# Kernel optimization log

Hardware: AMD Instinct MI355X
Metric: run time of the kernel (lower is better)

## Reference

```python
import jax, jax.numpy as jnp
import numpy as np

B, S, H = 1, 2048, 2048
NH, HD, RD = 32, 64, 64      # n_heads, head_dim, qk_mqa_dim (rope dim)
QR, KVR = 1024, 896          # q_lora_rank, kv_lora_rank
EPS = 1e-6
SCALE = HD ** -0.5           # scaling = head_dim ** -0.5 (as in module)


def rotate_half(x):
    x1, x2 = jnp.split(x, 2, axis=-1)
    return jnp.concatenate((-x2, x1), axis=-1)


def rmsnorm(x, w):
    var = jnp.mean(jnp.square(x), axis=-1, keepdims=True)
    return x * jax.lax.rsqrt(var + EPS) * w


def setup_inputs() -> dict:
    key = jax.random.key(0)
    ks = jax.random.split(key, 8)
    hidden_states = jax.random.normal(ks[0], (B, S, H), jnp.float32)
    # rotary tables over RD dims (applied only to the rope slice)
    inv_freq = 1.0 / (10000.0 ** (np.arange(0, RD, 2, dtype=np.float32) / RD))
    ang = np.arange(S, dtype=np.float32)[:, None] * inv_freq[None, :]
    emb = np.concatenate([ang, ang], axis=-1)  # [S, RD]
    cos = jnp.tile(jnp.asarray(np.cos(emb))[None], (B, 1, 1))
    sin = jnp.tile(jnp.asarray(np.sin(emb))[None], (B, 1, 1))
    s = 0.02
    q_a_w = s * jax.random.normal(ks[1], (QR, H), jnp.float32)
    q_a_ln_w = jnp.ones((QR,), jnp.float32)
    q_b_w = s * jax.random.normal(ks[2], (NH * (HD + RD), QR), jnp.float32)
    kv_a_w = s * jax.random.normal(ks[3], (KVR + RD, H), jnp.float32)
    kv_a_ln_w = jnp.ones((KVR,), jnp.float32)
    kv_b_w = s * jax.random.normal(ks[4], (NH * 2 * HD, KVR), jnp.float32)
    o_w = s * jax.random.normal(ks[5], (H, NH * HD), jnp.float32)
    return {"hidden_states": hidden_states, "cos": cos, "sin": sin,
            "q_a_w": q_a_w, "q_a_ln_w": q_a_ln_w, "q_b_w": q_b_w,
            "kv_a_w": kv_a_w, "kv_a_ln_w": kv_a_ln_w, "kv_b_w": kv_b_w,
            "o_w": o_w}


def reference(hidden_states, cos, sin, q_a_w, q_a_ln_w, q_b_w,
              kv_a_w, kv_a_ln_w, kv_b_w, o_w):
    b, s, _ = hidden_states.shape
    # Q: low-rank down -> RMSNorm -> up, split nope/rope per head
    q_lat = rmsnorm(hidden_states @ q_a_w.T, q_a_ln_w)             # [B,S,QR]
    q = (q_lat @ q_b_w.T).reshape(b, s, NH, HD + RD).transpose(0, 2, 1, 3)
    q_nope, q_rope = q[..., :HD], q[..., HD:]                      # [B,NH,S,HD/RD]
    # KV: joint down-proj with shared MQA rope key
    ckv = hidden_states @ kv_a_w.T                                 # [B,S,KVR+RD]
    c_kv, k_rope = ckv[..., :KVR], ckv[..., KVR:]
    k_rope = k_rope[:, None]                                       # [B,1,S,RD]
    kv = (rmsnorm(c_kv, kv_a_ln_w) @ kv_b_w.T).reshape(b, s, NH, 2 * HD)
    kv = kv.transpose(0, 2, 1, 3)                                  # [B,NH,S,2HD]
    k_nope, v = kv[..., :HD], kv[..., HD:]
    # RoPE on rope slices only (cos/sin unsqueezed over head dim)
    c_, s_ = cos[:, None], sin[:, None]
    q_rope = q_rope * c_ + rotate_half(q_rope) * s_
    k_rope = k_rope * c_ + rotate_half(k_rope) * s_
    q_full = jnp.concatenate([q_nope, q_rope], axis=-1)            # [B,NH,S,HD+RD]
    k_full = jnp.concatenate(
        [k_nope, jnp.broadcast_to(k_rope, (b, NH, s, RD))], axis=-1)
    # causal SDPA
    scores = jnp.einsum('bhqd,bhkd->bhqk', q_full, k_full) * SCALE
    mask = jnp.tril(jnp.ones((s, s), bool))
    scores = jnp.where(mask, scores, jnp.finfo(scores.dtype).min)
    attn = jax.nn.softmax(scores, axis=-1)
    out = jnp.einsum('bhqk,bhkd->bhqd', attn, v)                   # [B,NH,S,HD]
    out = out.transpose(0, 2, 1, 3).reshape(b, s, NH * HD)
    return out @ o_w.T                                             # [B,S,H]
```

## Files before the change

### kernel.cpp

```cpp
#include <hip/hip_runtime.h>


typedef __attribute__((ext_vector_type(8))) __bf16 bf16x8;
typedef __attribute__((ext_vector_type(4))) float f32x4;
typedef __attribute__((ext_vector_type(4))) unsigned u32x4;

__device__ __forceinline__ unsigned short f2bf(float f) {
  unsigned int x = __builtin_bit_cast(unsigned int, f);
  x += 0x7fffu + ((x >> 16) & 1u);
  return (unsigned short)(x >> 16);
}
__device__ __forceinline__ void gload_lds16(const void* g, void* l) {
  __builtin_amdgcn_global_load_lds(
      (const __attribute__((address_space(1))) void*)g,
      (__attribute__((address_space(3))) void*)l, 16, 0, 0);
}

struct CvtSegs {
  const float* src[6];
  unsigned short* dst[6];
  unsigned int n_src[6];
  unsigned int n_tot[6];
  unsigned int blk0[7];
};

__global__ __launch_bounds__(256) void cvt_all(CvtSegs sg) {
  int b = blockIdx.x;
  int seg = 0;
#pragma unroll
  for (int k = 0; k < 5; ++k)
    if (b >= (int)sg.blk0[k + 1]) seg = k + 1;
  size_t i = ((size_t)(b - sg.blk0[seg]) * 256 + threadIdx.x) * 4;
  if (i >= sg.n_tot[seg]) return;
  unsigned short o0 = 0, o1 = 0, o2 = 0, o3 = 0;
  if (i < sg.n_src[seg]) {
    float4 v = *reinterpret_cast<const float4*>(sg.src[seg] + i);
    o0 = f2bf(v.x); o1 = f2bf(v.y); o2 = f2bf(v.z); o3 = f2bf(v.w);
  }
  *reinterpret_cast<ushort4*>(sg.dst[seg] + i) = make_ushort4(o0, o1, o2, o3);
}

__global__ __launch_bounds__(512, 4) void gemm_bt2(const unsigned short* __restrict__ A,
                                                   const unsigned short* __restrict__ B,
                                                   float* __restrict__ C,
                                                   int M, int N, int K) {
  __shared__ unsigned short lA0[128 * 64], lA1[128 * 64];
  __shared__ unsigned short lB0[64 * 64], lB1[64 * 64];
  const int tid = threadIdx.x, lane = tid & 63, wv = tid >> 6;
  const int wr = wv >> 1, wc = wv & 1;
  const int bm = blockIdx.y * 128, bn = blockIdx.x * 64;

  f32x4 acc[2][2] = {};

  const int ar0 = tid >> 3;
  const int acol = (((tid & 7) ^ ((tid >> 3) & 7))) * 8;
  const int swz = lane & 7;

  auto stage = [&](unsigned short* la, unsigned short* lb, int k0) {
#pragma unroll
    for (int i = 0; i < 2; ++i)
      gload_lds16(A + (size_t)(bm + i * 64 + ar0) * K + k0 + acol,
                  &la[(i * 512 + wv * 64) * 8]);
    gload_lds16(B + (size_t)(bn + ar0) * K + k0 + acol, &lb[(wv * 64) * 8]);
  };

  auto compute = [&](const unsigned short* la, const unsigned short* lb) {
#pragma unroll
    for (int ks = 0; ks < 2; ++ks) {
      const int ch = ((ks * 4 + (lane >> 4)) ^ swz) * 8;
      bf16x8 af[2], bfr[2];
#pragma unroll
      for (int m = 0; m < 2; ++m)
        af[m] = *reinterpret_cast<const bf16x8*>(
            &la[(wr * 32 + m * 16 + (lane & 15)) * 64 + ch]);
#pragma unroll
      for (int n = 0; n < 2; ++n)
        bfr[n] = *reinterpret_cast<const bf16x8*>(
            &lb[(wc * 32 + n * 16 + (lane & 15)) * 64 + ch]);
      __builtin_amdgcn_s_setprio(1);
#pragma unroll
      for (int m = 0; m < 2; ++m)
#pragma unroll
        for (int n = 0; n < 2; ++n)
          acc[m][n] = __builtin_amdgcn_mfma_f32_16x16x32_bf16(af[m], bfr[n], acc[m][n], 0, 0, 0);
      __builtin_amdgcn_s_setprio(0);
    }
  };

  stage(lA0, lB0, 0);
  for (int k0 = 0; k0 < K; k0 += 128) {
    __syncthreads();
    stage(lA1, lB1, k0 + 64);
    compute(lA0, lB0);
    __syncthreads();
    if (k0 + 128 < K) stage(lA0, lB0, k0 + 128);
    compute(lA1, lB1);
  }

  const int r0 = bm + wr * 32, c0 = bn + wc * 32;
#pragma unroll
  for (int m = 0; m < 2; ++m)
#pragma unroll
    for (int n = 0; n < 2; ++n)
#pragma unroll
      for (int r = 0; r < 4; ++r)
        C[(size_t)(r0 + m * 16 + (lane >> 4) * 4 + r) * N + c0 + n * 16 + (lane & 15)] =
            acc[m][n][r];
}

__global__ __launch_bounds__(256) void rmsnorm_rope(const float* __restrict__ C1,
                                                    const float* __restrict__ qw,
                                                    const float* __restrict__ kvw,
                                                    const float* __restrict__ cosp,
                                                    const float* __restrict__ sinp,
                                                    unsigned short* __restrict__ qn,
                                                    unsigned short* __restrict__ ckvn,
                                                    unsigned short* __restrict__ kr) {
  const int s = blockIdx.x, tid = threadIdx.x;
  const float* row = C1 + (size_t)s * 2048;
  __shared__ float red[4];

  float4 v = *reinterpret_cast<const float4*>(row + tid * 4);
  float ss = v.x * v.x + v.y * v.y + v.z * v.z + v.w * v.w;
  ss += __shfl_xor(ss, 32); ss += __shfl_xor(ss, 16); ss += __shfl_xor(ss, 8);
  ss += __shfl_xor(ss, 4);  ss += __shfl_xor(ss, 2);  ss += __shfl_xor(ss, 1);
  if ((tid & 63) == 0) red[tid >> 6] = ss;
  __syncthreads();
  float rs = rsqrtf((red[0] + red[1] + red[2] + red[3]) * (1.f / 1024.f) + 1e-6f);
  {
    float4 w = *reinterpret_cast<const float4*>(qw + tid * 4);
    *reinterpret_cast<ushort4*>(qn + (size_t)s * 1024 + tid * 4) =
        make_ushort4(f2bf(v.x * rs * w.x), f2bf(v.y * rs * w.y),
                     f2bf(v.z * rs * w.z), f2bf(v.w * rs * w.w));
  }

  float4 u = make_float4(0.f, 0.f, 0.f, 0.f);
  if (tid < 224) u = *reinterpret_cast<const float4*>(row + 1024 + tid * 4);
  ss = u.x * u.x + u.y * u.y + u.z * u.z + u.w * u.w;
  ss += __shfl_xor(ss, 32); ss += __shfl_xor(ss, 16); ss += __shfl_xor(ss, 8);
  ss += __shfl_xor(ss, 4);  ss += __shfl_xor(ss, 2);  ss += __shfl_xor(ss, 1);
  __syncthreads();
  if ((tid & 63) == 0) red[tid >> 6] = ss;
  __syncthreads();
  rs = rsqrtf((red[0] + red[1] + red[2] + red[3]) * (1.f / 896.f) + 1e-6f);
  if (tid < 224) {
    float4 w = *reinterpret_cast<const float4*>(kvw + tid * 4);
    *reinterpret_cast<ushort4*>(ckvn + (size_t)s * 896 + tid * 4) =
        make_ushort4(f2bf(u.x * rs * w.x), f2bf(u.y * rs * w.y),
                     f2bf(u.z * rs * w.z), f2bf(u.w * rs * w.w));
  }

  if (tid < 64) {
    int d = tid;
    float x = row[1920 + d];
    float part = (d < 32) ? -row[1920 + d + 32] : row[1920 + d - 32];
    float vv = x * cosp[(size_t)s * 64 + d] + part * sinp[(size_t)s * 64 + d];
    kr[(size_t)s * 64 + d] = f2bf(vv);
  }
}

__global__ __launch_bounds__(256) void q_post(const float* __restrict__ Qf,
                                              const float* __restrict__ cosp,
                                              const float* __restrict__ sinp,
                                              unsigned short* __restrict__ Qb) {
  size_t base = ((size_t)blockIdx.x * 256 + threadIdx.x) * 4;
  int s = (int)(base >> 12);
  int w = (int)(base & 127);
  float4 x = *reinterpret_cast<const float4*>(Qf + base);
  float4 o;
  if (w < 64) {
    o = x;
  } else {
    int d = w - 64;
    float sgn = (d < 32) ? -1.f : 1.f;
    float4 prt = (d < 32) ? *reinterpret_cast<const float4*>(Qf + base + 32)
                          : *reinterpret_cast<const float4*>(Qf + base - 32);
    float4 c = *reinterpret_cast<const float4*>(cosp + (size_t)s * 64 + d);
    float4 sn = *reinterpret_cast<const float4*>(sinp + (size_t)s * 64 + d);
    o.x = x.x * c.x + sgn * prt.x * sn.x;
    o.y = x.y * c.y + sgn * prt.y * sn.y;
    o.z = x.z * c.z + sgn * prt.z * sn.z;
    o.w = x.w * c.w + sgn * prt.w * sn.w;
  }
  const float SC = 0.18033688f;
  *reinterpret_cast<ushort4*>(Qb + base) =
      make_ushort4(f2bf(o.x * SC), f2bf(o.y * SC), f2bf(o.z * SC), f2bf(o.w * SC));
}

__global__ __launch_bounds__(256) void kv_post(const float* __restrict__ KVf,
                                               const unsigned short* __restrict__ kr,
                                               unsigned short* __restrict__ Kb,
                                               unsigned short* __restrict__ Vt) {
  __shared__ float lT[64 * 65];
  const int s0 = blockIdx.x * 64, h = blockIdx.y, tid = threadIdx.x;
  for (int idx = tid; idx < 4096; idx += 256) {
    int r = idx >> 6, c = idx & 63;
    size_t base = (size_t)(s0 + r) * 4096 + h * 128;
    Kb[base + c] = f2bf(KVf[base + c]);
    Kb[base + 64 + c] = kr[(size_t)(s0 + r) * 64 + c];
    lT[r * 65 + c] = KVf[base + 64 + c];
  }
  __syncthreads();
  for (int idx = tid; idx < 4096; idx += 256) {
    int d = idx >> 6, c = idx & 63;
    Vt[((size_t)h * 64 + d) * 2048 + s0 + c] = f2bf(lT[c * 65 + d]);
  }
}

__global__ __launch_bounds__(256, 4) void flash_attn(const unsigned short* __restrict__ Qb,
                                                     const unsigned short* __restrict__ Kb,
                                                     const unsigned short* __restrict__ Vt,
                                                     unsigned short* __restrict__ Ao) {
  __shared__ unsigned short lK0[64 * 128], lK1[64 * 128];
  const int tid = threadIdx.x, lane = tid & 63, wv = tid >> 6;
  const int h = blockIdx.x;
  const int qb = (int)gridDim.y - 1 - (int)blockIdx.y;
  const int q0 = qb * 64;
  const int nt = qb + 1;
  const int firstrow = q0 + wv * 16;
  const int qa = firstrow + (lane & 15);

  bf16x8 qf[4];
  {
    const unsigned short* qrow = Qb + (size_t)(firstrow + (lane & 15)) * 4096 + h * 128;
#pragma unroll
    for (int ks = 0; ks < 4; ++ks)
      qf[ks] = *reinterpret_cast<const bf16x8*>(qrow + ks * 32 + (lane >> 4) * 8);
  }

  f32x4 o_acc[4] = {};
  float mrow = -1e30f, lrow = 0.f;

  const int g = lane >> 4;
  const int sl0 = ((g & 1) * 2) * 16 + (lane & 15);
  const int sl1 = sl0 + 16;
  const bool hi = g >= 2;

  const int krow = wv * 4 + (lane >> 4);
  const int kcol = (((lane & 15) ^ (krow & 7)) * 8);
  const int swz = lane & 7;

  auto stage = [&](int t, unsigned short* lK) {
    int j0 = t * 64;
#pragma unroll
    for (int i = 0; i < 4; ++i)
      gload_lds16(Kb + (size_t)(j0 + i * 16 + krow) * 4096 + h * 128 + kcol,
                  &lK[(i * 16 + wv * 4) * 128]);
  };

  auto loadV = [&](int j0, bf16x8 (&vr)[2][4]) {
#pragma unroll
    for (int ks = 0; ks < 2; ++ks)
#pragma unroll
      for (int n = 0; n < 4; ++n)
        vr[ks][n] = *reinterpret_cast<const bf16x8*>(
            Vt + ((size_t)h * 64 + n * 16 + (lane & 15)) * 2048 + j0 + ks * 32 +
            (lane >> 4) * 8);
  };

  auto computeT = [&](int j0, const unsigned short* lK, const bf16x8 (&vr)[2][4]) {
    f32x4 sT[4] = {};
    __builtin_amdgcn_s_setprio(1);
#pragma unroll
    for (int n = 0; n < 4; ++n)
#pragma unroll
      for (int ks = 0; ks < 4; ++ks) {
        bf16x8 kf = *reinterpret_cast<const bf16x8*>(
            &lK[(n * 16 + (lane & 15)) * 128 + (((ks * 4 + (lane >> 4)) ^ swz)) * 8]);
        sT[n] = __builtin_amdgcn_mfma_f32_16x16x32_bf16(kf, qf[ks], sT[n], 0, 0, 0);
      }
    __builtin_amdgcn_s_setprio(0);

    if (j0 == q0) {
#pragma unroll
      for (int n = 0; n < 4; ++n)
#pragma unroll
        for (int r = 0; r < 4; ++r) {
          int key = j0 + n * 16 + g * 4 + r;
          if (key > qa) sT[n][r] = -1e30f;
        }
    }

    float mx = sT[0][0];
#pragma unroll
    for (int n = 0; n < 4; ++n)
#pragma unroll
      for (int r = 0; r < 4; ++r) mx = fmaxf(mx, sT[n][r]);
    mx = fmaxf(mx, __shfl_xor(mx, 16));
    mx = fmaxf(mx, __shfl_xor(mx, 32));

    if (__any(mx - mrow > 8.0f)) {
      float mn = fmaxf(mrow, mx);
      float sf = exp2f(mrow - mn);
      mrow = mn;
      lrow *= sf;
      float sfr[4];
#pragma unroll
      for (int r = 0; r < 4; ++r) sfr[r] = __shfl(sf, (lane >> 4) * 4 + r);
#pragma unroll
      for (int n = 0; n < 4; ++n)
#pragma unroll
        for (int r = 0; r < 4; ++r) o_acc[n][r] *= sfr[r];
    }

    float ps = 0.f;
    unsigned dw[4][2];
#pragma unroll
    for (int n = 0; n < 4; ++n) {
      float p0 = exp2f(sT[n][0] - mrow), p1 = exp2f(sT[n][1] - mrow);
      float p2 = exp2f(sT[n][2] - mrow), p3 = exp2f(sT[n][3] - mrow);
      ps += (p0 + p1) + (p2 + p3);
      asm("v_cvt_pk_bf16_f32 %0, %1, %2" : "=v"(dw[n][0]) : "v"(p0), "v"(p1));
      asm("v_cvt_pk_bf16_f32 %0, %1, %2" : "=v"(dw[n][1]) : "v"(p2), "v"(p3));
    }
    ps += __shfl_xor(ps, 16);
    ps += __shfl_xor(ps, 32);
    lrow += ps;

#pragma unroll
    for (int ks = 0; ks < 2; ++ks) {
      unsigned A0 = __shfl(dw[2 * ks][0], sl0);
      unsigned B0 = __shfl(dw[2 * ks + 1][0], sl0);
      unsigned A1 = __shfl(dw[2 * ks][1], sl0);
      unsigned B1 = __shfl(dw[2 * ks + 1][1], sl0);
      unsigned A2 = __shfl(dw[2 * ks][0], sl1);
      unsigned B2 = __shfl(dw[2 * ks + 1][0], sl1);
      unsigned A3 = __shfl(dw[2 * ks][1], sl1);
      unsigned B3 = __shfl(dw[2 * ks + 1][1], sl1);
      u32x4 mm;
      mm.x = hi ? B0 : A0; mm.y = hi ? B1 : A1;
      mm.z = hi ? B2 : A2; mm.w = hi ? B3 : A3;
      bf16x8 pa = __builtin_bit_cast(bf16x8, mm);
      __builtin_amdgcn_s_setprio(1);
#pragma unroll
      for (int n = 0; n < 4; ++n)
        o_acc[n] = __builtin_amdgcn_mfma_f32_16x16x32_bf16(pa, vr[ks][n], o_acc[n], 0, 0, 0);
      __builtin_amdgcn_s_setprio(0);
    }
  };

  bf16x8 vr[2][4];
  stage(0, lK0);
  for (int t = 0; t < nt; t += 2) {
    __syncthreads();
    if (t + 1 < nt) stage(t + 1, lK1);
    loadV(t * 64, vr);
    computeT(t * 64, lK0, vr);
    if (t + 1 < nt) {
      __syncthreads();
      if (t + 2 < nt) stage(t + 2, lK0);
      loadV((t + 1) * 64, vr);
      computeT((t + 1) * 64, lK1, vr);
    }
  }

  float inv = 1.f / lrow;
  float invr[4];
#pragma unroll
  for (int r = 0; r < 4; ++r) invr[r] = __shfl(inv, (lane >> 4) * 4 + r);
#pragma unroll
  for (int n = 0; n < 4; ++n)
#pragma unroll
    for (int r = 0; r < 4; ++r) {
      float o = o_acc[n][r] * invr[r];
      Ao[(size_t)(firstrow + (lane >> 4) * 4 + r) * 2048 + h * 64 + n * 16 + (lane & 15)] =
          f2bf(o);
    }
}

extern "C" void kernel_launch(void* const* d_in, const int* in_sizes, int n_in,
                              void* d_out, int out_size, void* d_ws, size_t ws_size,
                              hipStream_t stream) {
  const float* hs   = (const float*)d_in[0];
  const float* cosp = (const float*)d_in[1];
  const float* sinp = (const float*)d_in[2];
  const float* qaw  = (const float*)d_in[3];
  const float* qaln = (const float*)d_in[4];
  const float* qbwf = (const float*)d_in[5];
  const float* kvaw = (const float*)d_in[6];
  const float* kvln = (const float*)d_in[7];
  const float* kvbwf= (const float*)d_in[8];
  const float* owf  = (const float*)d_in[9];
  float* out = (float*)d_out;
  char* ws = (char*)d_ws;
  const size_t MB = 1u << 20;

  unsigned short* W1b  = (unsigned short*)(ws + 0);
  unsigned short* Ao   = (unsigned short*)(ws + 0);
  unsigned short* qbw  = (unsigned short*)(ws + 8 * MB);
  unsigned short* Vt   = (unsigned short*)(ws + 8 * MB);
  unsigned short* kvbw = (unsigned short*)(ws + 16 * MB);
  unsigned short* owb  = (unsigned short*)(ws + 23 * MB);
  unsigned short* hsb  = (unsigned short*)(ws + 31 * MB);
  unsigned short* Qb   = (unsigned short*)(ws + 31 * MB);
  float*          C1   = (float*)(ws + 39 * MB);
  unsigned short* Kb   = (unsigned short*)(ws + 47 * MB);
  unsigned short* qln  = (unsigned short*)(ws + 55 * MB);
  unsigned short* ckvn = (unsigned short*)(ws + 59 * MB);
  unsigned short* kr   = (unsigned short*)(ws + 63 * MB);
  float*          Qf   = (float*)(ws + 64 * MB);
  float*          KVf  = (float*)(ws + 96 * MB);
  (void)ws_size; (void)in_sizes; (void)n_in; (void)out_size;

  CvtSegs sg;
  sg.src[0] = qaw;   sg.dst[0] = W1b;                      sg.n_src[0] = 1024u * 2048u; sg.n_tot[0] = 1024u * 2048u;
  sg.src[1] = kvaw;  sg.dst[1] = W1b + (size_t)1024 * 2048; sg.n_src[1] = 960u * 2048u;  sg.n_tot[1] = 1024u * 2048u;
  sg.src[2] = hs;    sg.dst[2] = hsb;                      sg.n_src[2] = 2048u * 2048u; sg.n_tot[2] = 2048u * 2048u;
  sg.src[3] = qbwf;  sg.dst[3] = qbw;                      sg.n_src[3] = 4096u * 1024u; sg.n_tot[3] = 4096u * 1024u;
  sg.src[4] = kvbwf; sg.dst[4] = kvbw;                     sg.n_src[4] = 4096u * 896u;  sg.n_tot[4] = 4096u * 896u;
  sg.src[5] = owf;   sg.dst[5] = owb;                      sg.n_src[5] = 2048u * 2048u; sg.n_tot[5] = 2048u * 2048u;
  sg.blk0[0] = 0;
  for (int k = 0; k < 6; ++k) sg.blk0[k + 1] = sg.blk0[k] + sg.n_tot[k] / 1024u;
  cvt_all<<<dim3(sg.blk0[6]), 256, 0, stream>>>(sg);

  gemm_bt2<<<dim3(32, 16), 512, 0, stream>>>(hsb, W1b, C1, 2048, 2048, 2048);
  rmsnorm_rope<<<2048, 256, 0, stream>>>(C1, qaln, kvln, cosp, sinp, qln, ckvn, kr);
  gemm_bt2<<<dim3(64, 16), 512, 0, stream>>>(qln, qbw, Qf, 2048, 4096, 1024);
  gemm_bt2<<<dim3(64, 16), 512, 0, stream>>>(ckvn, kvbw, KVf, 2048, 4096, 896);

  q_post<<<dim3((unsigned)(((size_t)2048 * 4096) / 1024)), 256, 0, stream>>>(Qf, cosp, sinp, Qb);
  kv_post<<<dim3(32, 32), 256, 0, stream>>>(KVf, kr, Kb, Vt);

  flash_attn<<<dim3(32, 32), 256, 0, stream>>>(Qb, Kb, Vt, Ao);

  gemm_bt2<<<dim3(32, 16), 512, 0, stream>>>(Ao, owb, out, 2048, 2048, 2048);
}
```

Baseline: 224.3 us.

## Split flash attention KV loop into two interleaved halves with a combine kernel

Each query block's KV tiles are now split between two workgroups by tile parity (even/odd), which doubles the grid to 2048 blocks. Each half writes unnormalized fp32 partial outputs plus per-row max and sum to workspace, and a new combine kernel merges them with rescaled softmax weights and emits bf16. The aim is more parallelism and better load balance in causal attention. The cost is an extra kernel launch, about 32 MB of fp32 partial writes and reads, and only single buffering of K per block instead of alternating tiles.

```diff
diff --git a/kernel.cpp b/kernel.cpp
--- a/kernel.cpp
+++ b/kernel.cpp
@@ -210,13 +210,14 @@
 __global__ __launch_bounds__(256, 4) void flash_attn(const unsigned short* __restrict__ Qb,
                                                      const unsigned short* __restrict__ Kb,
                                                      const unsigned short* __restrict__ Vt,
-                                                     unsigned short* __restrict__ Ao) {
+                                                     float* __restrict__ Op,
+                                                     float2* __restrict__ Ml) {
   __shared__ unsigned short lK0[64 * 128], lK1[64 * 128];
   const int tid = threadIdx.x, lane = tid & 63, wv = tid >> 6;
   const int h = blockIdx.x;
-  const int qb = (int)gridDim.y - 1 - (int)blockIdx.y;
+  const int qb = 31 - ((int)blockIdx.y >> 1);
+  const int j = (int)blockIdx.y & 1;
   const int q0 = qb * 64;
-  const int nt = qb + 1;
   const int firstrow = q0 + wv * 16;
   const int qa = firstrow + (lane & 15);
 
@@ -340,32 +341,47 @@
   };
 
   bf16x8 vr[2][4];
-  stage(0, lK0);
-  for (int t = 0; t < nt; t += 2) {
+  unsigned short* cur = lK0;
+  unsigned short* nxt = lK1;
+  if (j <= qb) stage(j, cur);
+  for (int t = j; t <= qb; t += 2) {
     __syncthreads();
-    if (t + 1 < nt) stage(t + 1, lK1);
+    if (t + 2 <= qb) stage(t + 2, nxt);
     loadV(t * 64, vr);
-    computeT(t * 64, lK0, vr);
-    if (t + 1 < nt) {
-      __syncthreads();
-      if (t + 2 < nt) stage(t + 2, lK0);
-      loadV((t + 1) * 64, vr);
-      computeT((t + 1) * 64, lK1, vr);
-    }
-  }
-
-  float inv = 1.f / lrow;
-  float invr[4];
-#pragma unroll
-  for (int r = 0; r < 4; ++r) invr[r] = __shfl(inv, (lane >> 4) * 4 + r);
+    computeT(t * 64, cur, vr);
+    unsigned short* tmp = cur; cur = nxt; nxt = tmp;
+  }
+
+  float* op = Op + (size_t)j * 4194304 + ((size_t)h * 2048 + firstrow) * 64;
 #pragma unroll
   for (int n = 0; n < 4; ++n)
 #pragma unroll
-    for (int r = 0; r < 4; ++r) {
-      float o = o_acc[n][r] * invr[r];
-      Ao[(size_t)(firstrow + (lane >> 4) * 4 + r) * 2048 + h * 64 + n * 16 + (lane & 15)] =
-          f2bf(o);
-    }
+    for (int r = 0; r < 4; ++r)
+      op[(size_t)(g * 4 + r) * 64 + n * 16 + (lane & 15)] = o_acc[n][r];
+  if (lane < 16)
+    Ml[(size_t)j * 65536 + h * 2048 + qa] = make_float2(mrow, lrow);
+}
+
+__global__ __launch_bounds__(256) void flash_combine(const float* __restrict__ Op,
+                                                     const float2* __restrict__ Ml,
+                                                     unsigned short* __restrict__ Ao) {
+  size_t i4 = ((size_t)blockIdx.x * 256 + threadIdx.x) * 4;
+  int s = (int)(i4 >> 11);
+  int c = (int)(i4 & 2047);
+  int h = c >> 6, d = c & 63;
+  float2 a = Ml[h * 2048 + s];
+  float2 b = Ml[65536 + h * 2048 + s];
+  float M = fmaxf(a.x, b.x);
+  float w0 = exp2f(a.x - M), w1 = exp2f(b.x - M);
+  float inv = 1.f / (w0 * a.y + w1 * b.y);
+  size_t pidx = ((size_t)h * 2048 + s) * 64 + d;
+  float4 o0 = *reinterpret_cast<const float4*>(Op + pidx);
+  float4 o1 = *reinterpret_cast<const float4*>(Op + 4194304 + pidx);
+  *reinterpret_cast<ushort4*>(Ao + (size_t)s * 2048 + h * 64 + d) =
+      make_ushort4(f2bf((w0 * o0.x + w1 * o1.x) * inv),
+                   f2bf((w0 * o0.y + w1 * o1.y) * inv),
+                   f2bf((w0 * o0.z + w1 * o1.z) * inv),
+                   f2bf((w0 * o0.w + w1 * o1.w) * inv));
 }
 
 extern "C" void kernel_launch(void* const* d_in, const int* in_sizes, int n_in,
@@ -400,6 +416,8 @@
   unsigned short* kr   = (unsigned short*)(ws + 63 * MB);
   float*          Qf   = (float*)(ws + 64 * MB);
   float*          KVf  = (float*)(ws + 96 * MB);
+  float*          Op   = (float*)(ws + 64 * MB);
+  float2*         Mlp  = (float2*)(ws + 98 * MB);
   (void)ws_size; (void)in_sizes; (void)n_in; (void)out_size;
 
   CvtSegs sg;
@@ -421,7 +439,8 @@
   q_post<<<dim3((unsigned)(((size_t)2048 * 4096) / 1024)), 256, 0, stream>>>(Qf, cosp, sinp, Qb);
   kv_post<<<dim3(32, 32), 256, 0, stream>>>(KVf, kr, Kb, Vt);
 
-  flash_attn<<<dim3(32, 32), 256, 0, stream>>>(Qb, Kb, Vt, Ao);
+  flash_attn<<<dim3(32, 64), 256, 0, stream>>>(Qb, Kb, Vt, Op, Mlp);
+  flash_combine<<<dim3(4096), 256, 0, stream>>>(Op, Mlp, Ao);
 
   gemm_bt2<<<dim3(32, 16), 512, 0, stream>>>(Ao, owb, out, 2048, 2048, 2048);
 }
```

After: 223.3 us. About the same (-0.4%).
